# Performance work log

Hardware: AMD Instinct MI355X
Metric: run time of the kernel (lower is better)

## Reference

```python
import jax, jax.numpy as jnp
import numpy as np

NUM_CLASSES = 1024
TAU = 1.0


def setup_inputs() -> dict:
    key = jax.random.key(0)
    k1, k2, k3 = jax.random.split(key, 3)
    N_s, N_q, D = 65536, 65536, 512
    z_support = jax.random.normal(k1, (N_s, D), dtype=jnp.float32)
    y_support = jax.random.randint(k2, (N_s,), 0, NUM_CLASSES, dtype=jnp.int64)
    z_query = jax.random.normal(k3, (N_q, D), dtype=jnp.float32)
    return {"z_support": z_support, "y_support": y_support, "z_query": z_query}


def reference(z_support, y_support, z_query):
    # Per-class mean prototypes via a single segment reduce.
    # (Assumes all classes 0..C-1 appear in y_support, so torch.unique remap is identity.)
    sums = jax.ops.segment_sum(z_support, y_support, num_segments=NUM_CLASSES)  # [C, D]
    counts = jax.ops.segment_sum(
        jnp.ones((z_support.shape[0],), dtype=z_support.dtype),
        y_support, num_segments=NUM_CLASSES)  # [C]
    protos = sums / jnp.maximum(counts, 1.0)[:, None]  # [C, D]

    # Pairwise squared euclidean: ||q||^2 + ||p||^2 - 2 q.p
    q_sq = jnp.sum(z_query * z_query, axis=-1, keepdims=True)          # [Nq, 1]
    p_sq = jnp.sum(protos * protos, axis=-1)[None, :]                  # [1, C]
    cross = jnp.einsum("nd,cd->nc", z_query, protos)                   # [Nq, C]
    dist = q_sq + p_sq - 2.0 * cross
    logits = -TAU * dist
    return logits
```

## Files before the change

### kernel.cpp

```cpp
#include <hip/hip_runtime.h>
#include <stdint.h>

#define C_CLASSES 1024
#define D_DIM     512
#define N_SUP     65536
#define N_QRY     65536
#define SLOTS     144

typedef float f32x4 __attribute__((ext_vector_type(4)));
typedef float f32x16v __attribute__((ext_vector_type(16)));
typedef short bf16x8 __attribute__((ext_vector_type(8)));
typedef unsigned short u16x4 __attribute__((ext_vector_type(4)));
typedef unsigned short u16x8 __attribute__((ext_vector_type(8)));

#define GLOBAL_AS __attribute__((address_space(1)))
#define LDS_AS    __attribute__((address_space(3)))

__device__ inline void async_copy16(const void* g, void* l) {
    __builtin_amdgcn_global_load_lds((const GLOBAL_AS void*)g, (LDS_AS void*)l, 16, 0, 0);
}

__device__ inline unsigned short f2bf(float f) {
    union { float f; unsigned int u; } x; x.f = f;
    unsigned int u = x.u;
    return (unsigned short)((u + 0x7fffu + ((u >> 16) & 1u)) >> 16);
}

template<bool CONV>
__global__ __launch_bounds__(256) void qsq_conv_kernel(
    const float* __restrict__ zq, float* __restrict__ qsq,
    unsigned short* __restrict__ Abf,
    const int* __restrict__ ys, int* __restrict__ cursors,
    int* __restrict__ rowlist)
{
    if (blockIdx.x < N_SUP / 256) {
        int i = blockIdx.x * 256 + threadIdx.x;
        int c = ys[i];
        int slot = atomicAdd(&cursors[c], 1);
        if (slot < SLOTS) rowlist[c * SLOTS + slot] = i;
    }

    const int w    = threadIdx.x >> 6;
    const int lane = threadIdx.x & 63;
    const int row  = blockIdx.x * 4 + w;
    const f32x4* zp = (const f32x4*)(zq + (size_t)row * D_DIM);
    f32x4 a = zp[2 * lane];
    f32x4 b = zp[2 * lane + 1];
    if (CONV) {
        u16x8 p;
        p.s0 = f2bf(a.x); p.s1 = f2bf(a.y); p.s2 = f2bf(a.z); p.s3 = f2bf(a.w);
        p.s4 = f2bf(b.x); p.s5 = f2bf(b.y); p.s6 = f2bf(b.z); p.s7 = f2bf(b.w);
        *(u16x8*)(Abf + (size_t)row * D_DIM + lane * 8) = p;
    }
    float s = a.x*a.x + a.y*a.y + a.z*a.z + a.w*a.w
            + b.x*b.x + b.y*b.y + b.z*b.z + b.w*b.w;
    #pragma unroll
    for (int off = 32; off > 0; off >>= 1) s += __shfl_down(s, off, 64);
    if (lane == 0) qsq[row] = s;
}

__global__ __launch_bounds__(256) void proto_gather(
    const float* __restrict__ zs, const int* __restrict__ rowlist,
    const int* __restrict__ cursors, unsigned short* __restrict__ protos,
    float* __restrict__ psq)
{
    const int c    = blockIdx.x;
    const int tid  = threadIdx.x;
    const int w    = tid >> 6;
    const int lane = tid & 63;

    const int cnt = cursors[c];
    const int m   = cnt < SLOTS ? cnt : SLOTS;

    __shared__ int sRows[SLOTS];
    if (tid < m) sRows[tid] = rowlist[c * SLOTS + tid];
    __syncthreads();

    f32x4 s0 = {0.f, 0.f, 0.f, 0.f};
    f32x4 s1 = {0.f, 0.f, 0.f, 0.f};
    int j = w;
    for (; j + 4 < m; j += 8) {
        int r0 = sRows[j];
        int r1 = sRows[j + 4];
        const f32x4* z0 = (const f32x4*)(zs + (size_t)r0 * D_DIM);
        const f32x4* z1 = (const f32x4*)(zs + (size_t)r1 * D_DIM);
        f32x4 a0 = z0[lane], a1 = z0[64 + lane];
        f32x4 b0 = z1[lane], b1 = z1[64 + lane];
        s0 += a0; s1 += a1;
        s0 += b0; s1 += b1;
    }
    for (; j < m; j += 4) {
        int r = sRows[j];
        const f32x4* zp = (const f32x4*)(zs + (size_t)r * D_DIM);
        s0 += zp[lane];
        s1 += zp[64 + lane];
    }

    __shared__ float sAcc[4][D_DIM];
    ((f32x4*)&sAcc[w][0])[lane]      = s0;
    ((f32x4*)&sAcc[w][0])[64 + lane] = s1;
    __syncthreads();

    float inv = 1.0f / fmaxf((float)cnt, 1.0f);
    int t2 = tid + 256;
    float p0 = (sAcc[0][tid] + sAcc[1][tid] + sAcc[2][tid] + sAcc[3][tid]) * inv;
    float p1 = (sAcc[0][t2]  + sAcc[1][t2]  + sAcc[2][t2]  + sAcc[3][t2])  * inv;
    protos[(size_t)c * D_DIM + tid] = f2bf(p0);
    protos[(size_t)c * D_DIM + t2]  = f2bf(p1);

    float ps = p0 * p0 + p1 * p1;
    #pragma unroll
    for (int off = 32; off > 0; off >>= 1) ps += __shfl_down(ps, off, 64);
    __shared__ float sPs[4];
    if (lane == 0) sPs[w] = ps;
    __syncthreads();
    if (tid == 0) psq[c] = sPs[0] + sPs[1] + sPs[2] + sPs[3];
}

__device__ __forceinline__ void stage_half(
    const unsigned short* __restrict__ src,
    unsigned short* dstTile,
    int rowBase,
    size_t gBase,
    int k0, int srow, int scg)
{
    async_copy16(src + (gBase + (size_t)(rowBase + srow)) * D_DIM + k0 + scg,
                 dstTile + (size_t)rowBase * 64);
}

__global__ __launch_bounds__(512, 2) void gemm256_kernel(
    const unsigned short* __restrict__ Abf,
    const unsigned short* __restrict__ Bp,
    const float* __restrict__ qsq, const float* __restrict__ psq,
    float* __restrict__ out)
{
    constexpr int BM = 256, BN = 256, BK = 64, K = D_DIM, NN = C_CLASSES;
    constexpr int NKT = K / BK;
    __shared__ __align__(16) unsigned short shA[2][BM * BK];
    __shared__ __align__(16) unsigned short shB[2][BN * BK];

    const int tid  = threadIdx.x;
    const int lane = tid & 63;
    const int w    = tid >> 6;
    const int wm   = w >> 2, wn = w & 3;
    const int l31  = lane & 31, half = lane >> 5;
    const int mBase = blockIdx.y * BM;
    const int nBase = blockIdx.x * BN;

    const int srow = lane >> 3;
    const int scg  = ((lane & 7) ^ srow) * 8;

    f32x16v acc[4][2];
    #pragma unroll
    for (int i = 0; i < 4; i++)
        #pragma unroll
        for (int j = 0; j < 2; j++)
            acc[i][j] = (f32x16v)(0.0f);

    #pragma unroll
    for (int t = 0; t < 2; t++) {
        int rb = (w * 2 + t) * 8;
        stage_half(Abf, &shA[0][0], rb,       mBase, 0, srow, scg);
        stage_half(Abf, &shA[0][0], 128 + rb, mBase, 0, srow, scg);
        stage_half(Bp,  &shB[0][0], rb,       nBase, 0, srow, scg);
        stage_half(Bp,  &shB[0][0], 128 + rb, nBase, 0, srow, scg);
    }
    asm volatile("s_waitcnt vmcnt(0)" ::: "memory");
    __builtin_amdgcn_s_barrier();

    for (int kt = 0; kt < NKT; ++kt) {
        const int kn = kt + 1;
        unsigned short* curA = &shA[kt & 1][0];
        unsigned short* curB = &shB[kt & 1][0];
        unsigned short* nxtA = &shA[kn & 1][0];
        unsigned short* nxtB = &shB[kn & 1][0];

        bf16x8 bfv[2][4];

        #pragma unroll
        for (int p = 0; p < 4; ++p) {
            bf16x8 af[4];
            const int ra = wm * 128 + p * 32 + l31;
            const int ga = ra & 7;
            #pragma unroll
            for (int ks = 0; ks < 4; ks++)
                af[ks] = *(const bf16x8*)&curA[ra * BK + (((ks * 2 + half) ^ ga) * 8)];
            if (p == 0) {
                #pragma unroll
                for (int n = 0; n < 2; n++) {
                    const int rb = wn * 64 + n * 32 + l31;
                    const int gb = rb & 7;
                    #pragma unroll
                    for (int ks = 0; ks < 4; ks++)
                        bfv[n][ks] = *(const bf16x8*)&curB[rb * BK + (((ks * 2 + half) ^ gb) * 8)];
                }
            }

            if (kn < NKT) {
                const unsigned short* srcT = (p < 2) ? Abf : Bp;
                unsigned short* dstT = (p < 2) ? nxtA : nxtB;
                const size_t gb = (p < 2) ? (size_t)mBase : (size_t)nBase;
                const int h = (p & 1) * 128;
                #pragma unroll
                for (int t = 0; t < 2; t++)
                    stage_half(srcT, dstT, h + (w * 2 + t) * 8, gb, kn * BK, srow, scg);
            }

            asm volatile("" ::: "memory");
            __builtin_amdgcn_s_barrier();

            __builtin_amdgcn_s_setprio(1);
            #pragma unroll
            for (int ks = 0; ks < 4; ks++)
                #pragma unroll
                for (int n = 0; n < 2; n++)
                    acc[p][n] = __builtin_amdgcn_mfma_f32_32x32x16_bf16(
                        af[ks], bfv[n][ks], acc[p][n], 0, 0, 0);
            __builtin_amdgcn_s_setprio(0);

            if (p == 3)
                asm volatile("s_waitcnt vmcnt(0) lgkmcnt(0)" ::: "memory");
            else
                asm volatile("s_waitcnt lgkmcnt(0)" ::: "memory");
            __builtin_amdgcn_s_barrier();
        }
    }

    const int rowb = mBase + wm * 128;
    const int colb = nBase + wn * 64;
    float pv[2];
    #pragma unroll
    for (int n = 0; n < 2; n++) pv[n] = psq[colb + n * 32 + l31];
    #pragma unroll
    for (int m = 0; m < 4; m++) {
        #pragma unroll
        for (int rg = 0; rg < 4; rg++) {
            int rbase = rowb + m * 32 + rg * 8 + half * 4;
            f32x4 qv = *(const f32x4*)&qsq[rbase];
            #pragma unroll
            for (int rr = 0; rr < 4; rr++) {
                int reg = rg * 4 + rr;
                size_t rowoff = (size_t)(rbase + rr) * NN;
                #pragma unroll
                for (int n = 0; n < 2; n++) {
                    out[rowoff + colb + n * 32 + l31] =
                        2.0f * acc[m][n][reg] - qv[rr] - pv[n];
                }
            }
        }
    }
}

__global__ __launch_bounds__(256) void gemm_kernel_slow(
    const float* __restrict__ A32,
    const unsigned short* __restrict__ Bp,
    const float* __restrict__ qsq, const float* __restrict__ psq,
    float* __restrict__ out)
{
    constexpr int BM = 128, BN = 128, BK = 64, K = D_DIM, NN = C_CLASSES;
    __shared__ __align__(16) unsigned short shA[BM * BK];
    __shared__ __align__(16) unsigned short shB[BN * BK];

    const int tid  = threadIdx.x;
    const int lane = tid & 63;
    const int w    = tid >> 6;
    const int wm   = w >> 1, wn = w & 1;
    const int l31  = lane & 31, half = lane >> 5;
    const int mBase = blockIdx.y * BM;
    const int nBase = blockIdx.x * BN;

    const int srow = lane >> 3;
    const int scg  = ((lane & 7) ^ srow) * 8;

    f32x16v acc[2][2];
    #pragma unroll
    for (int i = 0; i < 2; i++)
        #pragma unroll
        for (int j = 0; j < 2; j++)
            acc[i][j] = (f32x16v)(0.0f);

    for (int k0 = 0; k0 < K; k0 += BK) {
        __syncthreads();
        #pragma unroll
        for (int t = 0; t < 4; t++) {
            int q = tid * 4 + t;
            int r = q >> 3;
            int x = q & 7;
            int cg = x ^ (r & 7);
            const float* src = A32 + (size_t)(mBase + r) * K + k0 + cg * 8;
            f32x4 v0 = *(const f32x4*)src;
            f32x4 v1 = *(const f32x4*)(src + 4);
            u16x8 p;
            p.s0 = f2bf(v0.x); p.s1 = f2bf(v0.y); p.s2 = f2bf(v0.z); p.s3 = f2bf(v0.w);
            p.s4 = f2bf(v1.x); p.s5 = f2bf(v1.y); p.s6 = f2bf(v1.z); p.s7 = f2bf(v1.w);
            *(u16x8*)&shA[r * BK + x * 8] = p;
        }
        #pragma unroll
        for (int t = 0; t < 4; t++) {
            int g = w * 4 + t;
            async_copy16(Bp + (size_t)(nBase + g * 8 + srow) * K + k0 + scg,
                         &shB[g * 8 * BK]);
        }
        __syncthreads();

        bf16x8 af[2][4], bfv[2][4];
        #pragma unroll
        for (int i = 0; i < 2; i++) {
            int ra = wm * 64 + i * 32 + l31;
            int ga = ra & 7;
            int rb = wn * 64 + i * 32 + l31;
            int gb = rb & 7;
            #pragma unroll
            for (int ks = 0; ks < 4; ks++) {
                int c = ks * 2 + half;
                af[i][ks]  = *(const bf16x8*)&shA[ra * BK + ((c ^ ga) * 8)];
                bfv[i][ks] = *(const bf16x8*)&shB[rb * BK + ((c ^ gb) * 8)];
            }
        }
        #pragma unroll
        for (int ks = 0; ks < 4; ks++)
            #pragma unroll
            for (int i = 0; i < 2; i++)
                #pragma unroll
                for (int j = 0; j < 2; j++)
                    acc[i][j] = __builtin_amdgcn_mfma_f32_32x32x16_bf16(
                        af[i][ks], bfv[j][ks], acc[i][j], 0, 0, 0);
    }

    const int rowb = mBase + wm * 64;
    const int colb = nBase + wn * 64;
    float pv[2];
    #pragma unroll
    for (int j = 0; j < 2; j++) pv[j] = psq[colb + j * 32 + l31];
    #pragma unroll
    for (int i = 0; i < 2; i++) {
        #pragma unroll
        for (int rg = 0; rg < 4; rg++) {
            int rbase = rowb + i * 32 + rg * 8 + half * 4;
            f32x4 qv = *(const f32x4*)&qsq[rbase];
            #pragma unroll
            for (int rr = 0; rr < 4; rr++) {
                int reg = rg * 4 + rr;
                size_t rowoff = (size_t)(rbase + rr) * NN;
                #pragma unroll
                for (int j = 0; j < 2; j++) {
                    out[rowoff + colb + j * 32 + l31] =
                        2.0f * acc[i][j][reg] - qv[rr] - pv[j];
                }
            }
        }
    }
}

extern "C" void kernel_launch(void* const* d_in, const int* in_sizes, int n_in,
                              void* d_out, int out_size, void* d_ws, size_t ws_size,
                              hipStream_t stream) {
    const float* zs = (const float*)d_in[0];
    const int*   ys = (const int*)d_in[1];
    const float* zq = (const float*)d_in[2];
    float* out = (float*)d_out;

    const size_t szAbf     = (size_t)N_QRY * D_DIM * 2;
    const size_t szProtos  = (size_t)C_CLASSES * D_DIM * 2;
    const size_t szQsq     = (size_t)N_QRY * 4;
    const size_t szRowlist = (size_t)C_CLASSES * SLOTS * 4;
    const size_t szPsq     = 4096;
    const size_t szCur     = 4096;

    const size_t needFast = szAbf + szProtos + szQsq + szRowlist + szPsq + szCur;
    const bool fast = ws_size >= needFast;

    char* ws = (char*)d_ws;
    unsigned short* Abf = (unsigned short*)ws;
    char* base = fast ? ws + szAbf : ws;
    unsigned short* protos = (unsigned short*)base;
    float* qsq  = (float*)(base + szProtos);
    int*   rowlist = (int*)(base + szProtos + szQsq);
    float* psq  = (float*)(base + szProtos + szQsq + szRowlist);
    int*   cursors = (int*)(base + szProtos + szQsq + szRowlist + szPsq);

    hipMemsetAsync(cursors, 0, C_CLASSES * sizeof(int), stream);

    if (fast)
        qsq_conv_kernel<true><<<N_QRY / 4, 256, 0, stream>>>(
            zq, qsq, Abf, ys, cursors, rowlist);
    else
        qsq_conv_kernel<false><<<N_QRY / 4, 256, 0, stream>>>(
            zq, qsq, nullptr, ys, cursors, rowlist);
    proto_gather<<<C_CLASSES, 256, 0, stream>>>(zs, rowlist, cursors, protos, psq);
    if (fast)
        gemm256_kernel<<<dim3(C_CLASSES / 256, N_QRY / 256), 512, 0, stream>>>(
            Abf, protos, qsq, psq, out);
    else
        gemm_kernel_slow<<<dim3(C_CLASSES / 128, N_QRY / 128), 256, 0, stream>>>(
            zq, protos, qsq, psq, out);
}
```

Baseline: 541.1 us.

## Split scatter kernel, fuse prototype gather with query conversion, front-load GEMM staging

```diff
diff --git a/kernel.cpp b/kernel.cpp
--- a/kernel.cpp
+++ b/kernel.cpp
@@ -26,23 +26,80 @@
     return (unsigned short)((u + 0x7fffu + ((u >> 16) & 1u)) >> 16);
 }
 
-template<bool CONV>
-__global__ __launch_bounds__(256) void qsq_conv_kernel(
-    const float* __restrict__ zq, float* __restrict__ qsq,
-    unsigned short* __restrict__ Abf,
+__global__ __launch_bounds__(256) void scatter_kernel(
     const int* __restrict__ ys, int* __restrict__ cursors,
     int* __restrict__ rowlist)
 {
-    if (blockIdx.x < N_SUP / 256) {
-        int i = blockIdx.x * 256 + threadIdx.x;
-        int c = ys[i];
-        int slot = atomicAdd(&cursors[c], 1);
-        if (slot < SLOTS) rowlist[c * SLOTS + slot] = i;
-    }
-
-    const int w    = threadIdx.x >> 6;
-    const int lane = threadIdx.x & 63;
-    const int row  = blockIdx.x * 4 + w;
+    int i = blockIdx.x * 256 + threadIdx.x;
+    int c = ys[i];
+    int slot = atomicAdd(&cursors[c], 1);
+    if (slot < SLOTS) rowlist[c * SLOTS + slot] = i;
+}
+
+template<bool CONV>
+__global__ __launch_bounds__(256) void fused_qsq_gather(
+    const float* __restrict__ zq, float* __restrict__ qsq,
+    unsigned short* __restrict__ Abf,
+    const float* __restrict__ zs, const int* __restrict__ rowlist,
+    const int* __restrict__ cursors, unsigned short* __restrict__ protos,
+    float* __restrict__ psq)
+{
+    const int tid  = threadIdx.x;
+    const int w    = tid >> 6;
+    const int lane = tid & 63;
+
+    if (blockIdx.x < C_CLASSES) {
+        const int c   = blockIdx.x;
+        const int cnt = cursors[c];
+        const int m   = cnt < SLOTS ? cnt : SLOTS;
+
+        __shared__ int sRows[SLOTS];
+        if (tid < m) sRows[tid] = rowlist[c * SLOTS + tid];
+        __syncthreads();
+
+        f32x4 s0 = {0.f, 0.f, 0.f, 0.f};
+        f32x4 s1 = {0.f, 0.f, 0.f, 0.f};
+        int j = w;
+        for (; j + 4 < m; j += 8) {
+            int r0 = sRows[j];
+            int r1 = sRows[j + 4];
+            const f32x4* z0 = (const f32x4*)(zs + (size_t)r0 * D_DIM);
+            const f32x4* z1 = (const f32x4*)(zs + (size_t)r1 * D_DIM);
+            f32x4 a0 = z0[lane], a1 = z0[64 + lane];
+            f32x4 b0 = z1[lane], b1 = z1[64 + lane];
+            s0 += a0; s1 += a1;
+            s0 += b0; s1 += b1;
+        }
+        for (; j < m; j += 4) {
+            int r = sRows[j];
+            const f32x4* zp = (const f32x4*)(zs + (size_t)r * D_DIM);
+            s0 += zp[lane];
+            s1 += zp[64 + lane];
+        }
+
+        __shared__ float sAcc[4][D_DIM];
+        ((f32x4*)&sAcc[w][0])[lane]      = s0;
+        ((f32x4*)&sAcc[w][0])[64 + lane] = s1;
+        __syncthreads();
+
+        float inv = 1.0f / fmaxf((float)cnt, 1.0f);
+        int t2 = tid + 256;
+        float p0 = (sAcc[0][tid] + sAcc[1][tid] + sAcc[2][tid] + sAcc[3][tid]) * inv;
+        float p1 = (sAcc[0][t2]  + sAcc[1][t2]  + sAcc[2][t2]  + sAcc[3][t2])  * inv;
+        protos[(size_t)c * D_DIM + tid] = f2bf(p0);
+        protos[(size_t)c * D_DIM + t2]  = f2bf(p1);
+
+        float ps = p0 * p0 + p1 * p1;
+        #pragma unroll
+        for (int off = 32; off > 0; off >>= 1) ps += __shfl_down(ps, off, 64);
+        __shared__ float sPs[4];
+        if (lane == 0) sPs[w] = ps;
+        __syncthreads();
+        if (tid == 0) psq[c] = sPs[0] + sPs[1] + sPs[2] + sPs[3];
+        return;
+    }
+
+    const int row = (blockIdx.x - C_CLASSES) * 4 + w;
     const f32x4* zp = (const f32x4*)(zq + (size_t)row * D_DIM);
     f32x4 a = zp[2 * lane];
     f32x4 b = zp[2 * lane + 1];
@@ -57,64 +114,6 @@
     #pragma unroll
     for (int off = 32; off > 0; off >>= 1) s += __shfl_down(s, off, 64);
     if (lane == 0) qsq[row] = s;
-}
-
-__global__ __launch_bounds__(256) void proto_gather(
-    const float* __restrict__ zs, const int* __restrict__ rowlist,
-    const int* __restrict__ cursors, unsigned short* __restrict__ protos,
-    float* __restrict__ psq)
-{
-    const int c    = blockIdx.x;
-    const int tid  = threadIdx.x;
-    const int w    = tid >> 6;
-    const int lane = tid & 63;
-
-    const int cnt = cursors[c];
-    const int m   = cnt < SLOTS ? cnt : SLOTS;
-
-    __shared__ int sRows[SLOTS];
-    if (tid < m) sRows[tid] = rowlist[c * SLOTS + tid];
-    __syncthreads();
-
-    f32x4 s0 = {0.f, 0.f, 0.f, 0.f};
-    f32x4 s1 = {0.f, 0.f, 0.f, 0.f};
-    int j = w;
-    for (; j + 4 < m; j += 8) {
-        int r0 = sRows[j];
-        int r1 = sRows[j + 4];
-        const f32x4* z0 = (const f32x4*)(zs + (size_t)r0 * D_DIM);
-        const f32x4* z1 = (const f32x4*)(zs + (size_t)r1 * D_DIM);
-        f32x4 a0 = z0[lane], a1 = z0[64 + lane];
-        f32x4 b0 = z1[lane], b1 = z1[64 + lane];
-        s0 += a0; s1 += a1;
-        s0 += b0; s1 += b1;
-    }
-    for (; j < m; j += 4) {
-        int r = sRows[j];
-        const f32x4* zp = (const f32x4*)(zs + (size_t)r * D_DIM);
-        s0 += zp[lane];
-        s1 += zp[64 + lane];
-    }
-
-    __shared__ float sAcc[4][D_DIM];
-    ((f32x4*)&sAcc[w][0])[lane]      = s0;
-    ((f32x4*)&sAcc[w][0])[64 + lane] = s1;
-    __syncthreads();
-
-    float inv = 1.0f / fmaxf((float)cnt, 1.0f);
-    int t2 = tid + 256;
-    float p0 = (sAcc[0][tid] + sAcc[1][tid] + sAcc[2][tid] + sAcc[3][tid]) * inv;
-    float p1 = (sAcc[0][t2]  + sAcc[1][t2]  + sAcc[2][t2]  + sAcc[3][t2])  * inv;
-    protos[(size_t)c * D_DIM + tid] = f2bf(p0);
-    protos[(size_t)c * D_DIM + t2]  = f2bf(p1);
-
-    float ps = p0 * p0 + p1 * p1;
-    #pragma unroll
-    for (int off = 32; off > 0; off >>= 1) ps += __shfl_down(ps, off, 64);
-    __shared__ float sPs[4];
-    if (lane == 0) sPs[w] = ps;
-    __syncthreads();
-    if (tid == 0) psq[c] = sPs[0] + sPs[1] + sPs[2] + sPs[3];
 }
 
 __device__ __forceinline__ void stage_half(
@@ -196,14 +195,16 @@
                 }
             }
 
-            if (kn < NKT) {
-                const unsigned short* srcT = (p < 2) ? Abf : Bp;
-                unsigned short* dstT = (p < 2) ? nxtA : nxtB;
-                const size_t gb = (p < 2) ? (size_t)mBase : (size_t)nBase;
-                const int h = (p & 1) * 128;
-                #pragma unroll
-                for (int t = 0; t < 2; t++)
-                    stage_half(srcT, dstT, h + (w * 2 + t) * 8, gb, kn * BK, srow, scg);
+            if (kn < NKT && p < 2) {
+                const unsigned short* srcT = (p == 0) ? Abf : Bp;
+                unsigned short* dstT = (p == 0) ? nxtA : nxtB;
+                const size_t gb = (p == 0) ? (size_t)mBase : (size_t)nBase;
+                #pragma unroll
+                for (int t = 0; t < 2; t++) {
+                    int rb = (w * 2 + t) * 8;
+                    stage_half(srcT, dstT, rb,       gb, kn * BK, srow, scg);
+                    stage_half(srcT, dstT, 128 + rb, gb, kn * BK, srow, scg);
+                }
             }
 
             asm volatile("" ::: "memory");
@@ -381,13 +382,16 @@
 
     hipMemsetAsync(cursors, 0, C_CLASSES * sizeof(int), stream);
 
+    scatter_kernel<<<N_SUP / 256, 256, 0, stream>>>(ys, cursors, rowlist);
+
+    const int fusedGrid = C_CLASSES + N_QRY / 4;
     if (fast)
-        qsq_conv_kernel<true><<<N_QRY / 4, 256, 0, stream>>>(
-            zq, qsq, Abf, ys, cursors, rowlist);
+        fused_qsq_gather<true><<<fusedGrid, 256, 0, stream>>>(
+            zq, qsq, Abf, zs, rowlist, cursors, protos, psq);
     else
-        qsq_conv_kernel<false><<<N_QRY / 4, 256, 0, stream>>>(
-            zq, qsq, nullptr, ys, cursors, rowlist);
-    proto_gather<<<C_CLASSES, 256, 0, stream>>>(zs, rowlist, cursors, protos, psq);
+        fused_qsq_gather<false><<<fusedGrid, 256, 0, stream>>>(
+            zq, qsq, nullptr, zs, rowlist, cursors, protos, psq);
+
     if (fast)
         gemm256_kernel<<<dim3(C_CLASSES / 256, N_QRY / 256), 512, 0, stream>>>(
             Abf, protos, qsq, psq, out);
```

Result: no change. 535.7 us (-1.0%).
